# Optimization experiments

Measured on AMD Instinct MI355X. Metric: run time of the kernel, lower is better.

The kernel has to match this reference:

```python
import jax, jax.numpy as jnp
import numpy as np

N = 100000
E = 3200000
F_IN = 27
H1, C1 = 8, 8
H2, C2 = 1, 2
NEG_SLOPE = 0.2


def gat_conv(x, src, dst, W, a_src, a_dst, b, heads, ch, n_nodes):
    # x: [N, F_in]; src/dst: [E'] (self-loops already appended)
    h = (x @ W).reshape(n_nodes, heads, ch)            # [N, H, C]
    alpha_src = jnp.sum(h * a_src, axis=-1)            # [N, H]
    alpha_dst = jnp.sum(h * a_dst, axis=-1)            # [N, H]
    e = jax.nn.leaky_relu(alpha_src[src] + alpha_dst[dst], NEG_SLOPE)  # [E', H]
    m = jax.ops.segment_max(e, dst, num_segments=n_nodes)             # [N, H]
    ex = jnp.exp(e - m[dst])
    denom = jax.ops.segment_sum(ex, dst, num_segments=n_nodes)        # [N, H]
    alpha = ex / denom[dst]                                           # [E', H]
    out = jax.ops.segment_sum(h[src] * alpha[:, :, None], dst, num_segments=n_nodes)
    return out.reshape(n_nodes, heads * ch) + b


def setup_inputs() -> dict:
    key = jax.random.key(0)
    ks = jax.random.split(key, 10)
    x = jax.random.normal(ks[0], (N, F_IN), dtype=jnp.float32)
    edge_index = jax.random.randint(ks[1], (2, E), 0, N, dtype=jnp.int64)
    s1 = 1.0 / np.sqrt(F_IN)
    s2 = 1.0 / np.sqrt(H1 * C1)
    W1 = jax.random.uniform(ks[2], (F_IN, H1 * C1), jnp.float32, -s1, s1)
    a_src1 = jax.random.uniform(ks[3], (H1, C1), jnp.float32, -s1, s1)
    a_dst1 = jax.random.uniform(ks[4], (H1, C1), jnp.float32, -s1, s1)
    b1 = jnp.zeros((H1 * C1,), jnp.float32)
    W2 = jax.random.uniform(ks[5], (H1 * C1, H2 * C2), jnp.float32, -s2, s2)
    a_src2 = jax.random.uniform(ks[6], (H2, C2), jnp.float32, -s2, s2)
    a_dst2 = jax.random.uniform(ks[7], (H2, C2), jnp.float32, -s2, s2)
    b2 = jnp.zeros((H2 * C2,), jnp.float32)
    return {"x": x, "edge_index": edge_index, "W1": W1, "a_src1": a_src1,
            "a_dst1": a_dst1, "b1": b1, "W2": W2, "a_src2": a_src2,
            "a_dst2": a_dst2, "b2": b2}


def reference(x, edge_index, W1, a_src1, a_dst1, b1, W2, a_src2, a_dst2, b2):
    # eval mode: dropouts are identity. PyG GATConv adds self-loops by default.
    loop = jnp.arange(N, dtype=edge_index.dtype)
    src = jnp.concatenate([edge_index[0], loop])
    dst = jnp.concatenate([edge_index[1], loop])
    h = jax.nn.elu(gat_conv(x, src, dst, W1, a_src1, a_dst1, b1, H1, C1, N))
    out = gat_conv(h, src, dst, W2, a_src2, a_dst2, b2, H2, C2, N)
    return jax.nn.log_softmax(out, axis=1)
```

## Files before the change

kernel.cpp:

```cpp
#include <hip/hip_runtime.h>
#include <hip/hip_fp16.h>
#include <math.h>

#define NN 100000
#define EE 3200000
#define ET (EE + NN)

#define H1n 8
#define C1n 8
#define F1n 64
#define FINn 27
#define NEG 0.2f

#define NPB 128
#define NB 782
#define STRIDE 5120
#define TILE 4096
#define ABLK 256
#define WIN (STRIDE + NPB)

typedef float floatx2 __attribute__((ext_vector_type(2)));

static __device__ __forceinline__ float lrelu(float v) {
    return v > 0.f ? v : NEG * v;
}

__global__ __launch_bounds__(ABLK) void k_binA(const int* __restrict__ ei,
                                               int* __restrict__ tail,
                                               int* __restrict__ recs) {
    __shared__ int hist[NB];
    __shared__ int lofs[NB];
    __shared__ int cur[NB];
    __shared__ int gpos[NB];
    __shared__ int sorted[TILE];
    __shared__ unsigned short sbkt[TILE];
    __shared__ int part[ABLK];

    int tid = threadIdx.x;
    long long e0 = (long long)blockIdx.x * TILE;
    int cnt = (int)min((long long)TILE, (long long)EE - e0);

    for (int i = tid; i < NB; i += ABLK) hist[i] = 0;
    __syncthreads();

    int ss[TILE / ABLK], dd[TILE / ABLK];
    #pragma unroll
    for (int k = 0; k < TILE / ABLK; ++k) {
        int idx = k * ABLK + tid;
        if (idx < cnt) {
            ss[k] = ei[e0 + idx];
            dd[k] = ei[EE + e0 + idx];
            atomicAdd(&hist[dd[k] >> 7], 1);
        }
    }
    __syncthreads();
    {
        const int CH = (NB + ABLK - 1) / ABLK;
        int beg = tid * CH, end = min(beg + CH, NB);
        int s = 0;
        for (int i = beg; i < end; ++i) s += hist[i];
        part[tid] = s;
        __syncthreads();
        for (int off = 1; off < ABLK; off <<= 1) {
            int add = (tid >= off) ? part[tid - off] : 0;
            __syncthreads();
            part[tid] += add;
            __syncthreads();
        }
        int ex = (tid > 0) ? part[tid - 1] : 0;
        for (int i = beg; i < end; ++i) {
            lofs[i] = ex;
            cur[i] = ex;
            ex += hist[i];
        }
    }
    __syncthreads();
    #pragma unroll
    for (int k = 0; k < TILE / ABLK; ++k) {
        int idx = k * ABLK + tid;
        if (idx < cnt) {
            int b = dd[k] >> 7;
            int r = atomicAdd(&cur[b], 1);
            sorted[r] = ss[k] | ((dd[k] & (NPB - 1)) << 17);
            sbkt[r] = (unsigned short)b;
        }
    }
    __syncthreads();
    for (int i = tid; i < NB; i += ABLK) {
        int c = hist[i];
        if (c > 0) gpos[i] = atomicAdd(&tail[i], c);
    }
    __syncthreads();
    for (int t = tid; t < cnt; t += ABLK) {
        int b = sbkt[t];
        recs[(size_t)b * STRIDE + gpos[b] + (t - lofs[b])] = sorted[t];
    }
}

__global__ void k_bscan(const int* __restrict__ tail, int* __restrict__ bbase) {
    __shared__ int part[256];
    int tid = threadIdx.x;
    const int CH = (NB + 255) / 256;
    int beg = tid * CH, end = min(beg + CH, NB);
    int s = 0;
    for (int i = beg; i < end; ++i)
        s += tail[i] + min(NPB, NN - i * NPB);
    part[tid] = s;
    __syncthreads();
    for (int off = 1; off < 256; off <<= 1) {
        int add = (tid >= off) ? part[tid - off] : 0;
        __syncthreads();
        part[tid] += add;
        __syncthreads();
    }
    int ex = (tid > 0) ? part[tid - 1] : 0;
    for (int i = beg; i < end; ++i) {
        bbase[i] = ex;
        ex += tail[i] + min(NPB, NN - i * NPB);
    }
}

__global__ __launch_bounds__(128) void k_binB(const int* __restrict__ recs,
                                              const int* __restrict__ tail,
                                              const int* __restrict__ bbase,
                                              int* __restrict__ rowptr,
                                              int* __restrict__ csr) {
    __shared__ int hist[NPB];
    __shared__ int cur[NPB];
    __shared__ int window[WIN];
    __shared__ int wtot[2];

    int b = blockIdx.x;
    int tid = threadIdx.x;
    int node0 = b * NPB;
    int nodes = min(NPB, NN - node0);
    int cnt = tail[b];
    const int* rb = recs + (size_t)b * STRIDE;

    hist[tid] = 0;
    __syncthreads();
    for (int i = tid; i < cnt; i += 128) atomicAdd(&hist[rb[i] >> 17], 1);
    __syncthreads();
    int v = (tid < nodes) ? hist[tid] + 1 : 0;
    int inc = v;
    #pragma unroll
    for (int off = 1; off < 64; off <<= 1) {
        int t = __shfl_up(inc, off, 64);
        if ((tid & 63) >= off) inc += t;
    }
    if ((tid & 63) == 63) wtot[tid >> 6] = inc;
    __syncthreads();
    if (tid >= 64) inc += wtot[0];
    int T = wtot[0] + wtot[1];
    int ex = inc - v;
    int base = bbase[b];
    if (tid < nodes) {
        rowptr[node0 + tid] = base + ex;
        window[ex] = node0 + tid;
        cur[tid] = ex + 1;
    }
    if (b == NB - 1 && tid == 0) rowptr[NN] = base + T;
    __syncthreads();
    for (int i = tid; i < cnt; i += 128) {
        int r = rb[i];
        int p = atomicAdd(&cur[r >> 17], 1);
        window[p] = r & 0x1FFFF;
    }
    __syncthreads();
    for (int i = tid; i < T; i += 128) csr[base + i] = window[i];
}

__global__ __launch_bounds__(256) void k_h1(const float* __restrict__ x,
                                            const float* __restrict__ W1,
                                            const float* __restrict__ a_src1,
                                            const float* __restrict__ a_dst1,
                                            unsigned char* __restrict__ h1q,
                                            float* __restrict__ as1,
                                            float* __restrict__ ad1) {
    int gt = blockIdx.x * blockDim.x + threadIdx.x;
    int n = gt >> 6;
    if (n >= NN) return;
    int lane = threadIdx.x & 63;
    const float* xr = x + (size_t)n * FINn;
    float s = 0.f;
    #pragma unroll
    for (int k = 0; k < FINn; ++k) s = fmaf(xr[k], W1[k * F1n + lane], s);
    float s2 = __shfl_down(s, 1, 64);
    if (!(lane & 1)) {
        int pk = __builtin_amdgcn_cvt_pk_fp8_f32(s, s2, 0, false);
        ((unsigned short*)(h1q + (size_t)n * F1n))[lane >> 1] =
            (unsigned short)(pk & 0xFFFF);
    }
    float ps = s * a_src1[lane];
    float pd = s * a_dst1[lane];
    #pragma unroll
    for (int off = 1; off < 8; off <<= 1) {
        ps += __shfl_xor(ps, off, 64);
        pd += __shfl_xor(pd, off, 64);
    }
    if ((lane & 7) == 0) {
        int h = lane >> 3;
        as1[n * H1n + h] = ps;
        ad1[n * H1n + h] = pd;
    }
}

__global__ __launch_bounds__(256) void k_l1(const int* __restrict__ rowptr,
                                            const int* __restrict__ csr,
                                            const unsigned* __restrict__ h1q,
                                            const float* __restrict__ as1,
                                            const float* __restrict__ ad1,
                                            const float* __restrict__ b1,
                                            const float* __restrict__ W2,
                                            const float* __restrict__ a_src2,
                                            const float* __restrict__ a_dst2,
                                            float4* __restrict__ rec2) {
    int gt = blockIdx.x * blockDim.x + threadIdx.x;
    int n = gt >> 6;
    if (n >= NN) return;
    int lane = threadIdx.x & 63;
    int q = lane >> 4;
    int c4 = lane & 15;
    int h = c4 >> 1;
    float adh = ad1[(n << 3) + h];
    int beg = rowptr[n], end = rowptr[n + 1];
    float a0 = 0.f, a1 = 0.f, a2 = 0.f, a3 = 0.f, den = 0.f;

    #define QUAD(J)                                                          \
        {                                                                    \
            int t0 = __builtin_amdgcn_readlane(sidx, (J) + 0);               \
            int t1 = __builtin_amdgcn_readlane(sidx, (J) + 1);               \
            int t2 = __builtin_amdgcn_readlane(sidx, (J) + 2);               \
            int t3 = __builtin_amdgcn_readlane(sidx, (J) + 3);               \
            int sa = (q & 1) ? t1 : t0;                                      \
            int sb = (q & 1) ? t3 : t2;                                      \
            int s_ = (q & 2) ? sb : sa;                                      \
            float A_ = as1[(s_ << 3) + h];                                   \
            unsigned dw = h1q[((size_t)s_ << 4) + c4];                       \
            float e_ = A_ + adh;                                             \
            e_ = fmaxf(e_, 0.2f * e_);                                       \
            float x_ = ((J) + q < cnt) ? __expf(e_) : 0.f;                   \
            den += x_;                                                       \
            floatx2 lo = __builtin_amdgcn_cvt_pk_f32_fp8((int)dw, false);    \
            floatx2 hi = __builtin_amdgcn_cvt_pk_f32_fp8((int)dw, true);     \
            a0 = fmaf(x_, lo.x, a0);                                         \
            a1 = fmaf(x_, lo.y, a1);                                         \
            a2 = fmaf(x_, hi.x, a2);                                         \
            a3 = fmaf(x_, hi.y, a3);                                         \
        }

    for (int base = beg; base < end; base += 64) {
        int cnt = min(64, end - base);
        int sidx = (lane < cnt) ? csr[base + lane] : 0;
        for (int j = 0; j < cnt; j += 8) {
            QUAD(j)
            if (j + 4 < cnt) QUAD(j + 4)
        }
    }
    #undef QUAD

    #pragma unroll
    for (int off = 16; off < 64; off <<= 1) {
        a0 += __shfl_xor(a0, off, 64);
        a1 += __shfl_xor(a1, off, 64);
        a2 += __shfl_xor(a2, off, 64);
        a3 += __shfl_xor(a3, off, 64);
        den += __shfl_xor(den, off, 64);
    }
    float inv = 1.f / den;
    float v0 = a0 * inv + b1[c4 * 4 + 0];
    float v1 = a1 * inv + b1[c4 * 4 + 1];
    float v2 = a2 * inv + b1[c4 * 4 + 2];
    float v3 = a3 * inv + b1[c4 * 4 + 3];
    v0 = v0 > 0.f ? v0 : expm1f(v0);
    v1 = v1 > 0.f ? v1 : expm1f(v1);
    v2 = v2 > 0.f ? v2 : expm1f(v2);
    v3 = v3 > 0.f ? v3 : expm1f(v3);
    float p0 = v0 * W2[(c4 * 4 + 0) * 2 + 0] + v1 * W2[(c4 * 4 + 1) * 2 + 0] +
               v2 * W2[(c4 * 4 + 2) * 2 + 0] + v3 * W2[(c4 * 4 + 3) * 2 + 0];
    float p1 = v0 * W2[(c4 * 4 + 0) * 2 + 1] + v1 * W2[(c4 * 4 + 1) * 2 + 1] +
               v2 * W2[(c4 * 4 + 2) * 2 + 1] + v3 * W2[(c4 * 4 + 3) * 2 + 1];
    #pragma unroll
    for (int off = 1; off < 16; off <<= 1) {
        p0 += __shfl_xor(p0, off, 64);
        p1 += __shfl_xor(p1, off, 64);
    }
    if (lane == 0) {
        float4 r;
        r.x = p0;
        r.y = p1;
        r.z = p0 * a_src2[0] + p1 * a_src2[1];
        r.w = p0 * a_dst2[0] + p1 * a_dst2[1];
        rec2[n] = r;
    }
}

__global__ __launch_bounds__(256) void k_l2(const int* __restrict__ rowptr,
                                            const int* __restrict__ csr,
                                            const float4* __restrict__ rec2,
                                            const float* __restrict__ b2,
                                            float* __restrict__ out) {
    int gt = blockIdx.x * blockDim.x + threadIdx.x;
    int n = gt >> 6;
    if (n >= NN) return;
    int lane = threadIdx.x & 63;
    float adv = rec2[n].w;
    int beg = rowptr[n], end = rowptr[n + 1];
    float den = 0.f, a0 = 0.f, a1 = 0.f;
    for (int i = beg + lane; i < end; i += 64) {
        int s = csr[i];
        float4 r = rec2[s];
        float e = lrelu(r.z + adv);
        float ex = __expf(e);
        den += ex;
        a0 = fmaf(ex, r.x, a0);
        a1 = fmaf(ex, r.y, a1);
    }
    #pragma unroll
    for (int off = 32; off > 0; off >>= 1) {
        den += __shfl_xor(den, off, 64);
        a0 += __shfl_xor(a0, off, 64);
        a1 += __shfl_xor(a1, off, 64);
    }
    if (lane == 0) {
        float v0 = a0 / den + b2[0];
        float v1 = a1 / den + b2[1];
        float mx = fmaxf(v0, v1);
        float ls = mx + logf(__expf(v0 - mx) + __expf(v1 - mx));
        out[n * 2 + 0] = v0 - ls;
        out[n * 2 + 1] = v1 - ls;
    }
}

extern "C" void kernel_launch(void* const* d_in, const int* in_sizes, int n_in,
                              void* d_out, int out_size, void* d_ws, size_t ws_size,
                              hipStream_t stream) {
    const float* x      = (const float*)d_in[0];
    const int*   ei     = (const int*)d_in[1];
    const float* W1     = (const float*)d_in[2];
    const float* a_src1 = (const float*)d_in[3];
    const float* a_dst1 = (const float*)d_in[4];
    const float* b1     = (const float*)d_in[5];
    const float* W2     = (const float*)d_in[6];
    const float* a_src2 = (const float*)d_in[7];
    const float* a_dst2 = (const float*)d_in[8];
    const float* b2     = (const float*)d_in[9];
    float* out = (float*)d_out;

    char* wsb = (char*)d_ws;
    size_t o = 0;
    float4* rec2 = (float4*)wsb;                 o += (size_t)NN * 16;
    #define ALLOC(name, type, count) type* name = (type*)(wsb + o); o += (size_t)(count) * 4;
    ALLOC(as1,    float, NN * H1n)
    ALLOC(ad1,    float, NN * H1n)
    ALLOC(rowptr, int,   NN + 1)
    ALLOC(csr,    int,   ET)
    ALLOC(recs,   int,   (size_t)NB * STRIDE)
    ALLOC(tail,   int,   NB)
    ALLOC(bbase,  int,   NB)
    #undef ALLOC
    unsigned char* h1q = (unsigned char*)(wsb + o);  o += (size_t)NN * F1n;

    const int B = 256;
    #define GRID(n) ((unsigned)(((long long)(n) + B - 1) / B))

    hipMemsetAsync(tail, 0, (size_t)NB * sizeof(int), stream);
    k_binA<<<(EE + TILE - 1) / TILE, ABLK, 0, stream>>>(ei, tail, recs);
    k_bscan<<<1, 256, 0, stream>>>(tail, bbase);
    k_binB<<<NB, 128, 0, stream>>>(recs, tail, bbase, rowptr, csr);

    k_h1<<<GRID((size_t)NN * 64), B, 0, stream>>>(x, W1, a_src1, a_dst1, h1q, as1, ad1);

    k_l1<<<GRID((size_t)NN * 64), B, 0, stream>>>(rowptr, csr, (const unsigned*)h1q,
                                                  as1, ad1, b1, W2, a_src2, a_dst2, rec2);

    k_l2<<<GRID((size_t)NN * 64), B, 0, stream>>>(rowptr, csr, rec2, b2, out);
    #undef GRID
}
```

Baseline: 254.4 us.

## Store attention scores and layer-2 records in fp16; dedupe per-edge exp via bpermute

Source attention logits for layer 1 are stored as fp16, and the layer-2 per-node record shrinks from float4 to four packed halves (8 bytes). This halves the gather traffic on these arrays. In k_l1, the exp for each (edge, head) is now computed once, by lanes laid out as 8 edges x 8 heads, and passed to the feature lanes with ds_bpermute. Before, the 16 lanes sharing a head each recomputed it redundantly. The change adds cross-lane permutes and fp16 rounding error in the attention logits and the layer-2 features.

Measured after the change: 233.6 us. -8.2%, faster.

```diff
diff --git a/kernel.cpp b/kernel.cpp
--- a/kernel.cpp
+++ b/kernel.cpp
@@ -175,7 +175,7 @@
                                             const float* __restrict__ a_src1,
                                             const float* __restrict__ a_dst1,
                                             unsigned char* __restrict__ h1q,
-                                            float* __restrict__ as1,
+                                            __half* __restrict__ as1h,
                                             float* __restrict__ ad1) {
     int gt = blockIdx.x * blockDim.x + threadIdx.x;
     int n = gt >> 6;
@@ -200,7 +200,7 @@
     }
     if ((lane & 7) == 0) {
         int h = lane >> 3;
-        as1[n * H1n + h] = ps;
+        as1h[n * H1n + h] = __float2half(ps);
         ad1[n * H1n + h] = pd;
     }
 }
@@ -208,64 +208,68 @@
 __global__ __launch_bounds__(256) void k_l1(const int* __restrict__ rowptr,
                                             const int* __restrict__ csr,
                                             const unsigned* __restrict__ h1q,
-                                            const float* __restrict__ as1,
+                                            const __half* __restrict__ as1h,
                                             const float* __restrict__ ad1,
                                             const float* __restrict__ b1,
                                             const float* __restrict__ W2,
                                             const float* __restrict__ a_src2,
                                             const float* __restrict__ a_dst2,
-                                            float4* __restrict__ rec2) {
+                                            uint2* __restrict__ rec2) {
     int gt = blockIdx.x * blockDim.x + threadIdx.x;
     int n = gt >> 6;
     if (n >= NN) return;
     int lane = threadIdx.x & 63;
+    int e8 = lane >> 3;
+    int hh = lane & 7;
     int q = lane >> 4;
     int c4 = lane & 15;
-    int h = c4 >> 1;
-    float adh = ad1[(n << 3) + h];
+    float adh = ad1[(n << 3) + hh];
+    int bpe = e8 << 2;
+    int bpq = q << 2;
+    int bpx = ((q << 3) + (c4 >> 1)) << 2;
+
     int beg = rowptr[n], end = rowptr[n + 1];
     float a0 = 0.f, a1 = 0.f, a2 = 0.f, a3 = 0.f, den = 0.f;
-
-    #define QUAD(J)                                                          \
-        {                                                                    \
-            int t0 = __builtin_amdgcn_readlane(sidx, (J) + 0);               \
-            int t1 = __builtin_amdgcn_readlane(sidx, (J) + 1);               \
-            int t2 = __builtin_amdgcn_readlane(sidx, (J) + 2);               \
-            int t3 = __builtin_amdgcn_readlane(sidx, (J) + 3);               \
-            int sa = (q & 1) ? t1 : t0;                                      \
-            int sb = (q & 1) ? t3 : t2;                                      \
-            int s_ = (q & 2) ? sb : sa;                                      \
-            float A_ = as1[(s_ << 3) + h];                                   \
-            unsigned dw = h1q[((size_t)s_ << 4) + c4];                       \
-            float e_ = A_ + adh;                                             \
-            e_ = fmaxf(e_, 0.2f * e_);                                       \
-            float x_ = ((J) + q < cnt) ? __expf(e_) : 0.f;                   \
-            den += x_;                                                       \
-            floatx2 lo = __builtin_amdgcn_cvt_pk_f32_fp8((int)dw, false);    \
-            floatx2 hi = __builtin_amdgcn_cvt_pk_f32_fp8((int)dw, true);     \
-            a0 = fmaf(x_, lo.x, a0);                                         \
-            a1 = fmaf(x_, lo.y, a1);                                         \
-            a2 = fmaf(x_, hi.x, a2);                                         \
-            a3 = fmaf(x_, hi.y, a3);                                         \
-        }
 
     for (int base = beg; base < end; base += 64) {
         int cnt = min(64, end - base);
         int sidx = (lane < cnt) ? csr[base + lane] : 0;
-        for (int j = 0; j < cnt; j += 8) {
-            QUAD(j)
-            if (j + 4 < cnt) QUAD(j + 4)
-        }
-    }
-    #undef QUAD
-
+        for (int sb = 0; sb < cnt; sb += 8) {
+            int sb4 = sb << 2;
+            int s_sc = __builtin_amdgcn_ds_bpermute(sb4 + bpe, sidx);
+            float A = __half2float(as1h[((unsigned)s_sc << 3) + hh]);
+            float sc = A + adh;
+            sc = fmaxf(sc, 0.2f * sc);
+            float x = (sb + e8 < cnt) ? __expf(sc) : 0.f;
+            den += x;
+            int xi = __float_as_int(x);
+            #pragma unroll
+            for (int jj = 0; jj < 2; ++jj) {
+                int s_a = __builtin_amdgcn_ds_bpermute(sb4 + (jj << 4) + bpq, sidx);
+                int xr_ = __builtin_amdgcn_ds_bpermute((jj << 7) + bpx, xi);
+                float xv = __int_as_float(xr_);
+                unsigned dw = h1q[((unsigned)s_a << 4) + c4];
+                floatx2 lo = __builtin_amdgcn_cvt_pk_f32_fp8((int)dw, false);
+                floatx2 hi = __builtin_amdgcn_cvt_pk_f32_fp8((int)dw, true);
+                a0 = fmaf(xv, lo.x, a0);
+                a1 = fmaf(xv, lo.y, a1);
+                a2 = fmaf(xv, hi.x, a2);
+                a3 = fmaf(xv, hi.y, a3);
+            }
+        }
+    }
+
+    den += __shfl_xor(den, 8, 64);
+    den += __shfl_xor(den, 16, 64);
+    den += __shfl_xor(den, 32, 64);
+    den = __int_as_float(
+        __builtin_amdgcn_ds_bpermute((c4 >> 1) << 2, __float_as_int(den)));
     #pragma unroll
     for (int off = 16; off < 64; off <<= 1) {
         a0 += __shfl_xor(a0, off, 64);
         a1 += __shfl_xor(a1, off, 64);
         a2 += __shfl_xor(a2, off, 64);
         a3 += __shfl_xor(a3, off, 64);
-        den += __shfl_xor(den, off, 64);
     }
     float inv = 1.f / den;
     float v0 = a0 * inv + b1[c4 * 4 + 0];
@@ -286,35 +290,40 @@
         p1 += __shfl_xor(p1, off, 64);
     }
     if (lane == 0) {
-        float4 r;
-        r.x = p0;
-        r.y = p1;
-        r.z = p0 * a_src2[0] + p1 * a_src2[1];
-        r.w = p0 * a_dst2[0] + p1 * a_dst2[1];
+        float as2 = p0 * a_src2[0] + p1 * a_src2[1];
+        float ad2 = p0 * a_dst2[0] + p1 * a_dst2[1];
+        __half2 lo2 = __floats2half2_rn(p0, p1);
+        __half2 hi2 = __floats2half2_rn(as2, ad2);
+        uint2 r;
+        r.x = *(unsigned*)&lo2;
+        r.y = *(unsigned*)&hi2;
         rec2[n] = r;
     }
 }
 
 __global__ __launch_bounds__(256) void k_l2(const int* __restrict__ rowptr,
                                             const int* __restrict__ csr,
-                                            const float4* __restrict__ rec2,
+                                            const uint2* __restrict__ rec2,
                                             const float* __restrict__ b2,
                                             float* __restrict__ out) {
     int gt = blockIdx.x * blockDim.x + threadIdx.x;
     int n = gt >> 6;
     if (n >= NN) return;
     int lane = threadIdx.x & 63;
-    float adv = rec2[n].w;
+    __half2 mysd = *(const __half2*)&rec2[n].y;
+    float adv = __half2float(__high2half(mysd));
     int beg = rowptr[n], end = rowptr[n + 1];
     float den = 0.f, a0 = 0.f, a1 = 0.f;
     for (int i = beg + lane; i < end; i += 64) {
         int s = csr[i];
-        float4 r = rec2[s];
-        float e = lrelu(r.z + adv);
+        uint2 rv = rec2[s];
+        __half2 h01 = *(const __half2*)&rv.x;
+        __half2 hsd = *(const __half2*)&rv.y;
+        float e = lrelu(__half2float(__low2half(hsd)) + adv);
         float ex = __expf(e);
         den += ex;
-        a0 = fmaf(ex, r.x, a0);
-        a1 = fmaf(ex, r.y, a1);
+        a0 = fmaf(ex, __half2float(__low2half(h01)), a0);
+        a1 = fmaf(ex, __half2float(__high2half(h01)), a1);
     }
     #pragma unroll
     for (int off = 32; off > 0; off >>= 1) {
@@ -349,9 +358,8 @@
 
     char* wsb = (char*)d_ws;
     size_t o = 0;
-    float4* rec2 = (float4*)wsb;                 o += (size_t)NN * 16;
+    uint2* rec2 = (uint2*)wsb;                   o += (size_t)NN * 8;
     #define ALLOC(name, type, count) type* name = (type*)(wsb + o); o += (size_t)(count) * 4;
-    ALLOC(as1,    float, NN * H1n)
     ALLOC(ad1,    float, NN * H1n)
     ALLOC(rowptr, int,   NN + 1)
     ALLOC(csr,    int,   ET)
@@ -359,6 +367,7 @@
     ALLOC(tail,   int,   NB)
     ALLOC(bbase,  int,   NB)
     #undef ALLOC
+    __half* as1h = (__half*)(wsb + o);               o += (size_t)NN * H1n * 2;
     unsigned char* h1q = (unsigned char*)(wsb + o);  o += (size_t)NN * F1n;
 
     const int B = 256;
@@ -369,10 +378,10 @@
     k_bscan<<<1, 256, 0, stream>>>(tail, bbase);
     k_binB<<<NB, 128, 0, stream>>>(recs, tail, bbase, rowptr, csr);
 
-    k_h1<<<GRID((size_t)NN * 64), B, 0, stream>>>(x, W1, a_src1, a_dst1, h1q, as1, ad1);
+    k_h1<<<GRID((size_t)NN * 64), B, 0, stream>>>(x, W1, a_src1, a_dst1, h1q, as1h, ad1);
 
     k_l1<<<GRID((size_t)NN * 64), B, 0, stream>>>(rowptr, csr, (const unsigned*)h1q,
-                                                  as1, ad1, b1, W2, a_src2, a_dst2, rec2);
+                                                  as1h, ad1, b1, W2, a_src2, a_dst2, rec2);
 
     k_l2<<<GRID((size_t)NN * 64), B, 0, stream>>>(rowptr, csr, rec2, b2, out);
     #undef GRID
```
